# Optimization experiments

Measured on AMD Instinct MI355X. Metric: run time of the kernel, lower is better.

Reference implementation:

```python
import jax, jax.numpy as jnp
import numpy as np

N = 131072
E = 524288
H = 128
EPS = 1e-5

def _layernorm(h, g, b):
    mu = jnp.mean(h, axis=-1, keepdims=True)
    var = jnp.mean((h - mu) ** 2, axis=-1, keepdims=True)
    return (h - mu) * jax.lax.rsqrt(var + EPS) * g + b

def _node_to_node(x, senders, receivers, valid, num_nodes, params):
    # two-way (symmetrized) message passing: gather + scatter_add, then MLP+LN
    W1, b1, W2, b2, W3, b3, g, beta = params
    tws = jnp.concatenate([senders, receivers])
    twr = jnp.concatenate([receivers, senders])
    msg = x[tws]  # [2E', H] gather
    if valid is not None:
        msg = jnp.where(jnp.concatenate([valid, valid])[:, None], msg, 0.0)
    agg = jax.ops.segment_sum(msg, twr, num_segments=num_nodes)  # scatter_add
    h = jax.nn.gelu(agg @ W1 + b1, approximate=False)
    h = jax.nn.gelu(h @ W2 + b2, approximate=False)
    h = h @ W3 + b3
    return _layernorm(h, g, beta)

def setup_inputs() -> dict:
    key = jax.random.key(0)
    ks = jax.random.split(key, 20)
    s = 0.05
    inp = {
        "x": jax.random.normal(ks[0], (N, H), dtype=jnp.float32),
        "edge_index": jax.random.randint(ks[1], (2, E), 0, N, dtype=jnp.int32),
        "pool_p": jax.random.normal(ks[2], (H,), dtype=jnp.float32),
    }
    names = ["dW1", "db1", "dW2", "db2", "dW3", "db3", "dg", "dbeta",
             "uW1", "ub1", "uW2", "ub2", "uW3", "ub3", "ug", "ubeta"]
    shapes = [(H, H), (H,), (H, H), (H,), (H, H), (H,), (H,), (H,),
              (2 * H, H), (H,), (H, H), (H,), (H, H), (H,), (H,), (H,)]
    for i, (nm, sh) in enumerate(zip(names, shapes)):
        if nm in ("dg", "ug"):
            inp[nm] = jnp.ones(sh, dtype=jnp.float32)
        elif nm in ("dbeta", "ubeta") or nm.startswith(("db", "ub")):
            inp[nm] = jnp.zeros(sh, dtype=jnp.float32)
        else:
            inp[nm] = jax.random.normal(ks[3 + i], sh, dtype=jnp.float32) * s
    return inp

def reference(x, edge_index, pool_p,
              dW1, db1, dW2, db2, dW3, db3, dg, dbeta,
              uW1, ub1, uW2, ub2, uW3, ub3, ug, ubeta):
    senders, receivers = edge_index[0], edge_index[1]
    k = N // 2  # TopKPooling ratio=0.5

    # ---- down: TopKPooling ----
    score = x @ pool_p / jnp.linalg.norm(pool_p)  # [N]
    _, perm = jax.lax.top_k(score, k)             # kept node indices
    x_skip = x
    x_p = x[perm] * jnp.tanh(score[perm])[:, None]  # [k, H]
    mask = jnp.zeros((N,), dtype=bool).at[perm].set(True)
    mapping = jnp.zeros((N,), dtype=jnp.int32).at[perm].set(
        jnp.arange(k, dtype=jnp.int32))
    valid = mask[senders] & mask[receivers]
    ps, pr = mapping[senders], mapping[receivers]

    # down conv on pooled graph
    x_d = _node_to_node(x_p, ps, pr, valid, k,
                        (dW1, db1, dW2, db2, dW3, db3, dg, dbeta))

    # ---- up: unpool (indexed scatter write) + skip concat + up conv ----
    recovered = jnp.zeros_like(x_skip).at[perm].set(x_d)
    x_u = jnp.concatenate([recovered, x_skip], axis=-1)  # [N, 2H]
    out = _node_to_node(x_u, senders, receivers, None, N,
                        (uW1, ub1, uW2, ub2, uW3, ub3, ug, ubeta))
    return out
```

## Files before the change

kernel.cpp:

```cpp
#include <hip/hip_runtime.h>

#define N_NODES 131072
#define N_EDGES 524288
#define K_TOP   65536
#define LN_EPS  1e-5f
#define N_TILES (N_NODES / 64)
#define BCAP    5120u

typedef unsigned int u32;
typedef unsigned short u16;
typedef unsigned long long u64;

typedef __attribute__((ext_vector_type(8))) short bf8;
typedef __attribute__((ext_vector_type(4))) float f4;

#define ST_OFF    0
#define CANON_OFF (64u<<10)
#define PART_OFF  (576u<<10)
#define KEYS_OFF  (1u<<20)
#define TVAL_OFF  (2u<<20)
#define KEPT_OFF  ((2u<<20)+(512u<<10))
#define SBUF_OFF  (3u<<20)
#define ADJ_OFF   (35u<<20)


#define C_DW1 0
#define C_DB1 16384
#define C_DW2 16512
#define C_DB2 32896
#define C_DW3 33024
#define C_DB3 49408
#define C_DG  49536
#define C_DBE 49664
#define C_UW1 49792
#define C_UB1 82560
#define C_UW2 82688
#define C_UB2 99072
#define C_UW3 99200
#define C_UB3 115584
#define C_UG  115712
#define C_UBE 115840
#define C_TOT 115968
#define CT_DW1 115968
#define CT_DW2 132352
#define CT_DW3 148736
#define CT_UW1 165120
#define CT_UW2 197888
#define CT_UW3 214272
#define CT_TOT 230656

__device__ __forceinline__ float bflo(u32 u){ return __uint_as_float(u << 16); }
__device__ __forceinline__ float bfhi(u32 u){ return __uint_as_float(u & 0xFFFF0000u); }
__device__ __forceinline__ float bf2f(u16 v){ return __uint_as_float(((u32)v) << 16); }
__device__ __forceinline__ u32 f2bf(float f){
  u32 u = __float_as_uint(f);
  return (u + 0x7FFFu + ((u >> 16) & 1u)) >> 16;
}
__device__ __forceinline__ float gelu_f(float x){
  return 0.5f * x * (1.0f + erff(x * 0.7071067811865476f));
}
__device__ __forceinline__ float2 f2add(float2 a, float2 b){
  return make_float2(a.x + b.x, a.y + b.y);
}

__device__ __forceinline__ int swz16(int row, int cc){
  return row * 128 + ((cc ^ (row & 15)) * 8);
}

__device__ __forceinline__ bf8 ld_bf16_chunk(const u32* __restrict__ rowp, int s, int quad){
  uint4 v = *(const uint4*)(rowp + s * 16 + quad * 4);
  return __builtin_bit_cast(bf8, v);
}
__device__ __forceinline__ bf8 scale_bf16_chunk(const u32* __restrict__ rowp, int s, int quad, float tv){
  uint4 v = *(const uint4*)(rowp + s * 16 + quad * 4);
  uint4 q;
  q.x = f2bf(bflo(v.x) * tv) | (f2bf(bfhi(v.x) * tv) << 16);
  q.y = f2bf(bflo(v.y) * tv) | (f2bf(bfhi(v.y) * tv) << 16);
  q.z = f2bf(bflo(v.z) * tv) | (f2bf(bfhi(v.z) * tv) << 16);
  q.w = f2bf(bflo(v.w) * tv) | (f2bf(bfhi(v.w) * tv) << 16);
  return __builtin_bit_cast(bf8, q);
}
__device__ __forceinline__ bf8 cvt_f32_chunk(const float* __restrict__ rowp, int s, int quad, float tv){
  const float* p = rowp + s * 32 + quad * 8;
  float4 f0 = *(const float4*)p;
  float4 f1 = *(const float4*)(p + 4);
  uint4 q;
  q.x = f2bf(f0.x * tv) | (f2bf(f0.y * tv) << 16);
  q.y = f2bf(f0.z * tv) | (f2bf(f0.w * tv) << 16);
  q.z = f2bf(f1.x * tv) | (f2bf(f1.y * tv) << 16);
  q.w = f2bf(f1.z * tv) | (f2bf(f1.w * tv) << 16);
  return __builtin_bit_cast(bf8, q);
}

__device__ __forceinline__ void gemm_ab(const u16* ws, const bf8 a[4], int mn, int quad, f4 acc[8]){
  #pragma unroll
  for (int s = 0; s < 4; s++){
    #pragma unroll
    for (int j = 0; j < 8; j++){
      bf8 b = *(const bf8*)&ws[swz16(j * 16 + mn, s * 4 + quad)];
      acc[j] = __builtin_amdgcn_mfma_f32_16x16x32_bf16(a[s], b, acc[j], 0, 0, 0);
    }
  }
}

struct SelState {
  u64 prefix;
  u32 krem, eqcnt;
  int is_f32;
  u32 pad;
  double inv_norm;
  u32 eqlist[4096];
  u64 eqkey[4096];
};

struct P16 { const void* q[16]; };

__device__ __forceinline__ void chain_step(const u32* __restrict__ tots, int q,
                                           u32* sfx, u32* selb, int t,
                                           u64& pref, u32& target){
  sfx[t] = tots[q * 256 + t];
  __syncthreads();
  for (int o = 1; o < 256; o <<= 1){
    u32 x = (t + o < 256) ? sfx[t + o] : 0u;
    __syncthreads();
    sfx[t] += x;
    __syncthreads();
  }
  u32 above = (t == 255) ? 0u : sfx[t + 1];
  if (sfx[t] >= target && above < target){ selb[0] = (u32)t; selb[1] = target - above; }
  __syncthreads();
  pref = (pref << 8) | (u64)selb[0];
  target = selb[1];
  __syncthreads();
}

__global__ void k_detect(const u32* __restrict__ xw, SelState* st){
  int t = threadIdx.x;
  int cnt = 0;
  for (int i = t; i < 4096; i += 256){
    u32 w = xw[(size_t)i * 2048];
    u32 e = (w >> 23) & 0xFFu;
    if (e >= 97u && e <= 135u) cnt++;
  }
  __shared__ int sh[256];
  sh[t] = cnt; __syncthreads();
  for (int o = 128; o > 0; o >>= 1){ if (t < o) sh[t] += sh[t+o]; __syncthreads(); }
  if (t == 0){
    st->is_f32 = (sh[0] >= 3072) ? 1 : 0;
    st->prefix = 0; st->krem = K_TOP; st->eqcnt = 0;
  }
}

__global__ void k_canon(P16 ps, const SelState* __restrict__ st, u16* __restrict__ canon,
                        u32* __restrict__ tots, u32* __restrict__ gcur){
  int i = blockIdx.x * 256 + threadIdx.x;
  if (i < 1024) tots[i] = 0u;
  if (i < 256)  gcur[i] = (u32)i * BCAP;
  if (i >= CT_TOT) return;
  int isf = st->is_f32;
  if (i < C_TOT){
    const int off[17] = {C_DW1,C_DB1,C_DW2,C_DB2,C_DW3,C_DB3,C_DG,C_DBE,
                         C_UW1,C_UB1,C_UW2,C_UB2,C_UW3,C_UB3,C_UG,C_UBE,C_TOT};
    int seg = 0;
    #pragma unroll
    for (int s2 = 0; s2 < 16; s2++) if (i >= off[s2+1]) seg = s2 + 1;
    int j = i - off[seg];
    if (isf) canon[i] = (u16)f2bf(((const float*)ps.q[seg])[j]);
    else     canon[i] = ((const u16*)ps.q[seg])[j];
  } else {
    const int dst[7] = {CT_DW1, CT_DW2, CT_DW3, CT_UW1, CT_UW2, CT_UW3, CT_TOT};
    const int wq[6]  = {0, 2, 4, 8, 10, 12};
    int g = i;
    int seg = 0;
    #pragma unroll
    for (int s2 = 0; s2 < 6; s2++) if (g >= dst[s2+1]) seg = s2 + 1;
    int loc = g - dst[seg];
    int K = (seg == 3) ? 256 : 128;
    int n = loc / K, k = loc % K;
    int src = k * 128 + n;
    if (isf) canon[g] = (u16)f2bf(((const float*)ps.q[wq[seg]])[src]);
    else     canon[g] = ((const u16*)ps.q[wq[seg]])[src];
  }
}

__global__ __launch_bounds__(256) void k_score(const void* __restrict__ xraw, const void* __restrict__ praw,
                        const SelState* __restrict__ st,
                        u64* __restrict__ keys, float* __restrict__ tval){
  int t = threadIdx.x, lane = t & 63, w = t >> 6;
  int n = blockIdx.x * 4 + w;
  double d, ps;
  if (st->is_f32){
    const float* xf = (const float*)xraw + (size_t)n * 128;
    const float* pf = (const float*)praw;
    double p0 = (double)pf[lane], p1 = (double)pf[64 + lane];
    d  = (double)xf[lane] * p0 + (double)xf[64 + lane] * p1;
    ps = p0 * p0 + p1 * p1;
  } else {
    const u32* xw = (const u32*)xraw + (size_t)n * 64;
    const u32* pw = (const u32*)praw;
    u32 xx = xw[lane], pv = pw[lane];
    double p0 = (double)bflo(pv), p1 = (double)bfhi(pv);
    d  = (double)bflo(xx) * p0 + (double)bfhi(xx) * p1;
    ps = p0 * p0 + p1 * p1;
  }
  for (int o = 32; o > 0; o >>= 1){
    d  += __shfl_down(d,  o, 64);
    ps += __shfl_down(ps, o, 64);
  }
  if (lane == 0){
    double sc = d * (1.0 / sqrt(ps));
    u64 u = (u64)__double_as_longlong(sc);
    u64 key = (u & 0x8000000000000000ULL) ? ~u : (u | 0x8000000000000000ULL);
    keys[n] = key;
    tval[n] = tanhf((float)sc);
  }
}

__global__ __launch_bounds__(256) void k_histp(const u64* __restrict__ keys,
                                               u32* __restrict__ tots, int pass){
  __shared__ u32 sfx[256];
  __shared__ u32 selb[2];
  __shared__ u32 h[256];
  int t = threadIdx.x;
  u64 pref = 0;
  u32 target = K_TOP;
  for (int q = 0; q < pass; q++)
    chain_step(tots, q, sfx, selb, t, pref, target);
  h[t] = 0;
  __syncthreads();
  int sh_d = 56 - 8 * pass;
  for (int n = blockIdx.x * 256 + t; n < N_NODES; n += 256 * 256){
    u64 k = keys[n];
    bool m = (pass == 0) ? true : ((k >> (sh_d + 8)) == pref);
    if (m) atomicAdd(&h[(u32)((k >> sh_d) & 255)], 1u);
  }
  __syncthreads();
  if (h[t]) atomicAdd(&tots[pass * 256 + t], h[t]);
}

__global__ __launch_bounds__(256) void k_mark(const u64* __restrict__ keys,
                                              const u32* __restrict__ tots,
                                              SelState* st, u32* __restrict__ kept){
  __shared__ u32 sfx[256];
  __shared__ u32 selb[2];
  int t = threadIdx.x;
  u64 pref = 0;
  u32 target = K_TOP;
  for (int q = 0; q < 4; q++)
    chain_step(tots, q, sfx, selb, t, pref, target);
  u32 T = (u32)pref;
  int n = blockIdx.x * 256 + t;
  u64 k = keys[n];
  u32 t32 = (u32)(k >> 32);
  kept[n] = (t32 > T) ? 1u : 0u;
  if (t32 == T){
    u32 i = atomicAdd(&st->eqcnt, 1u);
    if (i < 4096){ st->eqlist[i] = (u32)n; st->eqkey[i] = k; }
  }
}

__global__ __launch_bounds__(256) void k_tie(const u32* __restrict__ tots,
                                             SelState* st, u32* __restrict__ kept){
  __shared__ u32 sfx[256];
  __shared__ u32 selb[2];
  int t = threadIdx.x;
  u64 pref = 0;
  u32 target = K_TOP;
  for (int q = 0; q < 4; q++)
    chain_step(tots, q, sfx, selb, t, pref, target);
  u32 r = target;
  u32 m = st->eqcnt; if (m > 4096) m = 4096;
  for (u32 i = t; i < m; i += 256){
    u64 ki = st->eqkey[i]; u32 ii = st->eqlist[i];
    u32 rank = 0;
    for (u32 j = 0; j < m; j++){
      u64 kj = st->eqkey[j];
      rank += (kj > ki || (kj == ki && st->eqlist[j] < ii)) ? 1u : 0u;
    }
    if (rank < r) kept[ii] = 1u;
  }
}

__global__ __launch_bounds__(256) void k_bin(const int* __restrict__ se, const int* __restrict__ re,
                                             u32* __restrict__ gcur, u32* __restrict__ pairs){
  __shared__ u32 cnt[256], sc[256], base[256], cur[256], gpos[256];
  __shared__ u32 stage[8192];
  int t = threadIdx.x;
  cnt[t] = 0;
  __syncthreads();
  int e0 = blockIdx.x * 4096;
  for (int i = t; i < 4096; i += 256){
    int s = se[e0 + i], r = re[e0 + i];
    atomicAdd(&cnt[(u32)r >> 9], 1u);
    atomicAdd(&cnt[(u32)s >> 9], 1u);
  }
  __syncthreads();
  sc[t] = cnt[t];
  __syncthreads();
  for (int o = 1; o < 256; o <<= 1){
    u32 x = (t >= o) ? sc[t - o] : 0u;
    __syncthreads();
    sc[t] += x;
    __syncthreads();
  }
  base[t] = sc[t] - cnt[t];
  cur[t] = base[t];
  gpos[t] = atomicAdd(&gcur[t], cnt[t]);
  __syncthreads();
  for (int i = t; i < 4096; i += 256){
    u32 s = (u32)se[e0 + i], r = (u32)re[e0 + i];
    u32 b1 = r >> 9, p1 = ((r & 511u) << 17) | s;
    u32 b2 = s >> 9, p2 = ((s & 511u) << 17) | r;
    stage[atomicAdd(&cur[b1], 1u)] = p1;
    stage[atomicAdd(&cur[b2], 1u)] = p2;
  }
  __syncthreads();
  int lane = t & 63, wv = t >> 6;
  for (int b = wv; b < 256; b += 4){
    u32 n = cnt[b], src = base[b], dst = gpos[b];
    for (u32 i = lane; i < n; i += 64)
      pairs[dst + i] = stage[src + i];
  }
}

__global__ __launch_bounds__(256) void k_place(const u32* __restrict__ gcur,
                                               const u32* __restrict__ pairs,
                                               const u32* __restrict__ kept,
                                               u32* __restrict__ adj,
                                               u32* __restrict__ off, u32* __restrict__ cnts){
  __shared__ u32 cnt[512], ck[512], curk[512], curn[512], lo[512], ex2[256];
  int b = blockIdx.x, t = threadIdx.x;
  u32 base = (u32)b * BCAP;
  u32 total = gcur[b] - base;
  cnt[t] = 0; cnt[t + 256] = 0;
  ck[t] = 0;  ck[t + 256] = 0;
  curk[t] = 0; curk[t + 256] = 0;
  curn[t] = 0; curn[t + 256] = 0;
  __syncthreads();
  for (u32 i = t; i < total; i += 256){
    u32 p = pairs[base + i];
    u32 nl = p >> 17, m = p & 0x1FFFFu;
    atomicAdd(&cnt[nl], 1u);
    if (kept[m]) atomicAdd(&ck[nl], 1u);
  }
  __syncthreads();
  u32 c0 = cnt[2 * t], c1 = cnt[2 * t + 1];
  ex2[t] = c0 + c1;
  __syncthreads();
  for (int o = 1; o < 256; o <<= 1){
    u32 x = (t >= o) ? ex2[t - o] : 0u;
    __syncthreads();
    ex2[t] += x;
    __syncthreads();
  }
  u32 e0 = ex2[t] - c0 - c1;
  int n0 = b * 512 + 2 * t;
  off[n0]     = base + e0;
  off[n0 + 1] = base + e0 + c0;
  cnts[n0]     = (ck[2 * t] << 16) | c0;
  cnts[n0 + 1] = (ck[2 * t + 1] << 16) | c1;
  lo[2 * t] = e0; lo[2 * t + 1] = e0 + c0;
  __syncthreads();
  for (u32 i = t; i < total; i += 256){
    u32 p = pairs[base + i];
    u32 nl = p >> 17, m = p & 0x1FFFFu;
    u32 slot;
    if (kept[m]) slot = base + lo[nl] + atomicAdd(&curk[nl], 1u);
    else         slot = base + lo[nl] + ck[nl] + atomicAdd(&curn[nl], 1u);
    adj[slot] = m;
  }
}


__global__ __launch_bounds__(256, 3) void k_proj_down(
    const void* __restrict__ xraw, const float* __restrict__ tval,
    const u16* __restrict__ W1T, const SelState* __restrict__ st,
    const u32* __restrict__ kept, u32* __restrict__ S)
{
  __shared__ u16 w1s[128 * 128];
  __shared__ u16 os[64 * 128];
  int t = threadIdx.x, lane = t & 63, wv = t >> 6;
  int m0 = wv * 16, mn = lane & 15, quad = lane >> 4;

  for (int i = t; i < 2048; i += 256){
    int row = i >> 4, cc = i & 15;
    *(uint4*)&w1s[swz16(row, cc)] = *(const uint4*)(W1T + row * 128 + cc * 8);
  }
  int isf = st->is_f32;
  __syncthreads();

  for (int tile = blockIdx.x; tile < N_TILES; tile += gridDim.x){
    int row0 = tile * 64;
    int arow = row0 + m0 + mn;
    float tv = tval[arow];
    bf8 a[4];
    if (isf){
      const float* xf = (const float*)xraw + (size_t)arow * 128;
      #pragma unroll
      for (int s = 0; s < 4; s++) a[s] = cvt_f32_chunk(xf, s, quad, tv);
    } else {
      const u32* xw = (const u32*)xraw + (size_t)arow * 64;
      #pragma unroll
      for (int s = 0; s < 4; s++) a[s] = scale_bf16_chunk(xw, s, quad, tv);
    }
    f4 acc[8];
    #pragma unroll
    for (int j = 0; j < 8; j++){ acc[j][0]=0.f; acc[j][1]=0.f; acc[j][2]=0.f; acc[j][3]=0.f; }
    gemm_ab(w1s, a, mn, quad, acc);

    #pragma unroll
    for (int j = 0; j < 8; j++){
      int c = j * 16 + mn;
      #pragma unroll
      for (int rg = 0; rg < 4; rg++){
        int row = m0 + quad * 4 + rg;
        os[row * 128 + ((c >> 3) ^ (row & 15)) * 8 + (c & 7)] = (u16)f2bf(acc[j][rg]);
      }
    }
    __builtin_amdgcn_wave_barrier();
    int rl = m0 + (lane >> 2), qt = lane & 3;
    u32 kp = kept[row0 + rl];
    u32* out = S + (size_t)(row0 + rl) * 64;
    if (kp){
      #pragma unroll
      for (int i = 0; i < 4; i++){
        int cc = qt * 4 + i;
        *(uint4*)(out + cc * 4) = *(const uint4*)&os[swz16(rl, cc)];
      }
    }
    __builtin_amdgcn_wave_barrier();
  }
}

__global__ __launch_bounds__(256, 2) void k_proj_up(
    const u32* __restrict__ R, const void* __restrict__ xraw,
    const u16* __restrict__ W1T, const SelState* __restrict__ st,
    u32* __restrict__ S2)
{
  __shared__ u16 was[128 * 128];
  __shared__ u16 wbs[128 * 128];
  __shared__ u16 os[64 * 128];
  int t = threadIdx.x, lane = t & 63, wv = t >> 6;
  int m0 = wv * 16, mn = lane & 15, quad = lane >> 4;

  for (int i = t; i < 2048; i += 256){
    int row = i >> 4, cc = i & 15;
    *(uint4*)&was[swz16(row, cc)] = *(const uint4*)(W1T + row * 256 + cc * 8);
    *(uint4*)&wbs[swz16(row, cc)] = *(const uint4*)(W1T + row * 256 + 128 + cc * 8);
  }
  int isf = st->is_f32;
  __syncthreads();

  for (int tile = blockIdx.x; tile < N_TILES; tile += gridDim.x){
    int row0 = tile * 64;
    int arow = row0 + m0 + mn;
    bf8 a[4];
    const u32* rp = R + (size_t)arow * 64;
    #pragma unroll
    for (int s = 0; s < 4; s++) a[s] = ld_bf16_chunk(rp, s, quad);
    f4 acc[8];
    #pragma unroll
    for (int j = 0; j < 8; j++){ acc[j][0]=0.f; acc[j][1]=0.f; acc[j][2]=0.f; acc[j][3]=0.f; }
    gemm_ab(was, a, mn, quad, acc);

    if (isf){
      const float* xf = (const float*)xraw + (size_t)arow * 128;
      #pragma unroll
      for (int s = 0; s < 4; s++) a[s] = cvt_f32_chunk(xf, s, quad, 1.0f);
    } else {
      const u32* xw = (const u32*)xraw + (size_t)arow * 64;
      #pragma unroll
      for (int s = 0; s < 4; s++) a[s] = ld_bf16_chunk(xw, s, quad);
    }
    gemm_ab(wbs, a, mn, quad, acc);

    #pragma unroll
    for (int j = 0; j < 8; j++){
      int c = j * 16 + mn;
      #pragma unroll
      for (int rg = 0; rg < 4; rg++){
        int row = m0 + quad * 4 + rg;
        os[row * 128 + ((c >> 3) ^ (row & 15)) * 8 + (c & 7)] = (u16)f2bf(acc[j][rg]);
      }
    }
    __builtin_amdgcn_wave_barrier();
    int rl = m0 + (lane >> 2), qt = lane & 3;
    u32* out = S2 + (size_t)(row0 + rl) * 64;
    #pragma unroll
    for (int i = 0; i < 4; i++){
      int cc = qt * 4 + i;
      *(uint4*)(out + cc * 4) = *(const uint4*)&os[swz16(rl, cc)];
    }
    __builtin_amdgcn_wave_barrier();
  }
}

template<int IS_DOWN>
__global__ __launch_bounds__(256, 4) void k_agg(
    const u32* __restrict__ Smsg, const u32* __restrict__ off, const u32* __restrict__ cnts,
    const u32* __restrict__ adj,
    const u16* __restrict__ cb1, const u32* __restrict__ kept,
    u32* __restrict__ H)
{
  int t = threadIdx.x, lane = t & 63, wv = t >> 6;
  float b1l = bf2f(cb1[2 * lane]), b1h = bf2f(cb1[2 * lane + 1]);
  int base = blockIdx.x * 16 + wv * 4;
  #pragma unroll 1
  for (int rr = 0; rr < 4; rr++){
    int n = base + rr;
    if (IS_DOWN && !kept[n]){ H[(size_t)n * 64 + lane] = 0u; continue; }
    u32 c = cnts[n];
    u32 jb = off[n];
    u32 je = jb + (IS_DOWN ? (c >> 16) : (c & 0xFFFFu));
    float2 a = make_float2(0.f, 0.f);
    u32 j = jb;
    for (; j + 8 <= je; j += 8){
      u32 e0 = adj[j],   e1 = adj[j+1], e2 = adj[j+2], e3 = adj[j+3];
      u32 e4 = adj[j+4], e5 = adj[j+5], e6 = adj[j+6], e7 = adj[j+7];
      u32 w0 = Smsg[(size_t)e0 * 64 + lane];
      u32 w1 = Smsg[(size_t)e1 * 64 + lane];
      u32 w2 = Smsg[(size_t)e2 * 64 + lane];
      u32 w3 = Smsg[(size_t)e3 * 64 + lane];
      u32 w4 = Smsg[(size_t)e4 * 64 + lane];
      u32 w5 = Smsg[(size_t)e5 * 64 + lane];
      u32 w6 = Smsg[(size_t)e6 * 64 + lane];
      u32 w7 = Smsg[(size_t)e7 * 64 + lane];
      float2 v0 = make_float2(bflo(w0), bfhi(w0));
      float2 v1 = make_float2(bflo(w1), bfhi(w1));
      float2 v2 = make_float2(bflo(w2), bfhi(w2));
      float2 v3 = make_float2(bflo(w3), bfhi(w3));
      float2 v4 = make_float2(bflo(w4), bfhi(w4));
      float2 v5 = make_float2(bflo(w5), bfhi(w5));
      float2 v6 = make_float2(bflo(w6), bfhi(w6));
      float2 v7 = make_float2(bflo(w7), bfhi(w7));
      a = f2add(a, f2add(f2add(f2add(v0, v1), f2add(v2, v3)),
                         f2add(f2add(v4, v5), f2add(v6, v7))));
    }
    for (; j + 4 <= je; j += 4){
      u32 e0 = adj[j], e1 = adj[j+1], e2 = adj[j+2], e3 = adj[j+3];
      u32 w0 = Smsg[(size_t)e0 * 64 + lane];
      u32 w1 = Smsg[(size_t)e1 * 64 + lane];
      u32 w2 = Smsg[(size_t)e2 * 64 + lane];
      u32 w3 = Smsg[(size_t)e3 * 64 + lane];
      float2 v0 = make_float2(bflo(w0), bfhi(w0));
      float2 v1 = make_float2(bflo(w1), bfhi(w1));
      float2 v2 = make_float2(bflo(w2), bfhi(w2));
      float2 v3 = make_float2(bflo(w3), bfhi(w3));
      a = f2add(a, f2add(f2add(v0, v1), f2add(v2, v3)));
    }
    for (; j < je; j++){
      u32 w = Smsg[(size_t)adj[j] * 64 + lane];
      a = f2add(a, make_float2(bflo(w), bfhi(w)));
    }
    H[(size_t)n * 64 + lane] = f2bf(gelu_f(a.x + b1l)) | (f2bf(gelu_f(a.y + b1h)) << 16);
  }
}

template<int IS_DOWN>
__global__ __launch_bounds__(256, 2) void k_mlp(
    const u32* __restrict__ H,
    const u16* __restrict__ cW2T, const u16* __restrict__ cb2,
    const u16* __restrict__ cW3T, const u16* __restrict__ cb3,
    const u16* __restrict__ cg, const u16* __restrict__ cbe,
    const u32* __restrict__ kept, const SelState* __restrict__ st,
    u32* __restrict__ Rout, void* __restrict__ fout)
{
  __shared__ u16 w2s[128 * 128];
  __shared__ u16 w3s[128 * 128];
  __shared__ u16 os[64 * 128];
  int t = threadIdx.x, lane = t & 63, wv = t >> 6;
  int m0 = wv * 16, mn = lane & 15, quad = lane >> 4;

  for (int i = t; i < 2048; i += 256){
    int row = i >> 4, cc = i & 15;
    *(uint4*)&w2s[swz16(row, cc)] = *(const uint4*)(cW2T + row * 128 + cc * 8);
    *(uint4*)&w3s[swz16(row, cc)] = *(const uint4*)(cW3T + row * 128 + cc * 8);
  }
  float b2v[8], b3v[8], gv[8], bev[8];
  #pragma unroll
  for (int j = 0; j < 8; j++){
    int c = j * 16 + mn;
    b2v[j] = bf2f(cb2[c]); b3v[j] = bf2f(cb3[c]);
    gv[j]  = bf2f(cg[c]);  bev[j] = bf2f(cbe[c]);
  }
  int isf = st->is_f32;
  __syncthreads();

  for (int tile = blockIdx.x; tile < N_TILES; tile += gridDim.x){
    int row0 = tile * 64;
    int arow = row0 + m0 + mn;

    bf8 a[4];
    const u32* hp = H + (size_t)arow * 64;
    #pragma unroll
    for (int s = 0; s < 4; s++) a[s] = ld_bf16_chunk(hp, s, quad);
    f4 acc[8];
    #pragma unroll
    for (int j = 0; j < 8; j++){ acc[j][0]=0.f; acc[j][1]=0.f; acc[j][2]=0.f; acc[j][3]=0.f; }
    gemm_ab(w2s, a, mn, quad, acc);

    #pragma unroll
    for (int j = 0; j < 8; j++){
      int c = j * 16 + mn;
      #pragma unroll
      for (int rg = 0; rg < 4; rg++){
        int row = m0 + quad * 4 + rg;
        os[row * 128 + ((c >> 3) ^ (row & 15)) * 8 + (c & 7)] = (u16)f2bf(gelu_f(acc[j][rg] + b2v[j]));
      }
    }
    __builtin_amdgcn_wave_barrier();

    #pragma unroll
    for (int s = 0; s < 4; s++) a[s] = *(const bf8*)&os[swz16(m0 + mn, s * 4 + quad)];
    #pragma unroll
    for (int j = 0; j < 8; j++){ acc[j][0]=0.f; acc[j][1]=0.f; acc[j][2]=0.f; acc[j][3]=0.f; }
    gemm_ab(w3s, a, mn, quad, acc);

    #pragma unroll
    for (int j = 0; j < 8; j++){
      #pragma unroll
      for (int rg = 0; rg < 4; rg++) acc[j][rg] += b3v[j];
    }
    float s1[4] = {0.f,0.f,0.f,0.f}, s2[4] = {0.f,0.f,0.f,0.f};
    #pragma unroll
    for (int j = 0; j < 8; j++){
      #pragma unroll
      for (int rg = 0; rg < 4; rg++){
        float v = acc[j][rg];
        s1[rg] += v; s2[rg] += v * v;
      }
    }
    #pragma unroll
    for (int o = 1; o < 16; o <<= 1){
      #pragma unroll
      for (int rg = 0; rg < 4; rg++){
        s1[rg] += __shfl_xor(s1[rg], o, 64);
        s2[rg] += __shfl_xor(s2[rg], o, 64);
      }
    }
    float mu[4], rs[4];
    #pragma unroll
    for (int rg = 0; rg < 4; rg++){
      mu[rg] = s1[rg] * 0.0078125f;
      float var = s2[rg] * 0.0078125f - mu[rg] * mu[rg];
      rs[rg] = rsqrtf(var + LN_EPS);
    }
    #pragma unroll
    for (int j = 0; j < 8; j++){
      #pragma unroll
      for (int rg = 0; rg < 4; rg++)
        acc[j][rg] = (acc[j][rg] - mu[rg]) * rs[rg] * gv[j] + bev[j];
    }

    if (!IS_DOWN && isf){
      float* fo = (float*)fout;
      #pragma unroll
      for (int j = 0; j < 8; j++){
        #pragma unroll
        for (int rg = 0; rg < 4; rg++)
          fo[(size_t)(row0 + m0 + quad * 4 + rg) * 128 + j * 16 + mn] = acc[j][rg];
      }
      continue;
    }

    __builtin_amdgcn_wave_barrier();
    #pragma unroll
    for (int j = 0; j < 8; j++){
      int c = j * 16 + mn;
      #pragma unroll
      for (int rg = 0; rg < 4; rg++){
        int row = m0 + quad * 4 + rg;
        os[row * 128 + ((c >> 3) ^ (row & 15)) * 8 + (c & 7)] = (u16)f2bf(acc[j][rg]);
      }
    }
    __builtin_amdgcn_wave_barrier();
    int rl = m0 + (lane >> 2), qt = lane & 3;
    u32 kp = IS_DOWN ? kept[row0 + rl] : 1u;
    u32* out = (IS_DOWN ? Rout : (u32*)fout) + (size_t)(row0 + rl) * 64;
    #pragma unroll
    for (int i = 0; i < 4; i++){
      int cc = qt * 4 + i;
      uint4 w = *(const uint4*)&os[swz16(rl, cc)];
      if (!kp){ w.x = 0; w.y = 0; w.z = 0; w.w = 0; }
      *(uint4*)(out + cc * 4) = w;
    }
    __builtin_amdgcn_wave_barrier();
  }
}


extern "C" void kernel_launch(void* const* d_in, const int* in_sizes, int n_in,
                              void* d_out, int out_size, void* d_ws, size_t ws_size,
                              hipStream_t stream)
{
  const void* x     = d_in[0];
  const int* eidx   = (const int*)d_in[1];
  const void* poolp = d_in[2];
  const int* senders = eidx;
  const int* receivers = eidx + N_EDGES;

  char* ws = (char*)d_ws;
  SelState* st = (SelState*)(ws + ST_OFF);
  u16*  canon  = (u16*) (ws + CANON_OFF);
  u32*  tots   = (u32*) (ws + PART_OFF);
  u32*  gcur   = (u32*) (ws + PART_OFF + 4096);
  u64*  keys   = (u64*) (ws + KEYS_OFF);
  u32*  off    = (u32*) (ws + KEYS_OFF);
  u32*  cnts   = (u32*) (ws + KEYS_OFF + (512u<<10));
  float* tval  = (float*)(ws + TVAL_OFF);
  u32*  kept   = (u32*) (ws + KEPT_OFF);
  u32*  Sbuf   = (u32*) (ws + SBUF_OFF);
  u32*  adj    = (u32*) (ws + ADJ_OFF);
  u32*  pairs  = Sbuf;
  u32*  Dbuf   = (u32*) d_out;

  P16 ps;
  for (int i = 0; i < 16; i++) ps.q[i] = d_in[3 + i];

  k_detect<<<1, 256, 0, stream>>>((const u32*)x, st);
  k_canon<<<(CT_TOT + 255) / 256, 256, 0, stream>>>(ps, st, canon, tots, gcur);
  k_score<<<N_NODES / 4, 256, 0, stream>>>(x, poolp, st, keys, tval);
  for (int pass = 0; pass < 4; pass++)
    k_histp<<<256, 256, 0, stream>>>(keys, tots, pass);
  k_mark<<<N_NODES / 256, 256, 0, stream>>>(keys, tots, st, kept);
  k_tie<<<1, 256, 0, stream>>>(tots, st, kept);

  k_bin<<<N_EDGES / 4096, 256, 0, stream>>>(senders, receivers, gcur, pairs);
  k_place<<<256, 256, 0, stream>>>(gcur, pairs, kept, adj, off, cnts);

  k_proj_down<<<768, 256, 0, stream>>>(x, tval, canon + CT_DW1, st, kept, Sbuf);
  k_agg<1><<<N_NODES / 16, 256, 0, stream>>>(Sbuf, off, cnts, adj, canon + C_DB1, kept, Dbuf);
  k_mlp<1><<<512, 256, 0, stream>>>(Dbuf,
      canon + CT_DW2, canon + C_DB2, canon + CT_DW3, canon + C_DB3,
      canon + C_DG, canon + C_DBE, kept, st, Sbuf, nullptr);

  k_proj_up<<<512, 256, 0, stream>>>(Sbuf, x, canon + CT_UW1, st, Dbuf);
  k_agg<0><<<N_NODES / 16, 256, 0, stream>>>(Dbuf, off, cnts, adj, canon + C_UB1, kept, Sbuf);
  k_mlp<0><<<512, 256, 0, stream>>>(Sbuf,
      canon + CT_UW2, canon + C_UB2, canon + CT_UW3, canon + C_UB3,
      canon + C_UG, canon + C_UBE, kept, st, nullptr, d_out);
}
```

Before: 441.7 us.

## Compact kept nodes into perm list and run down-path only on kept rows

Builds an explicit list of kept node indices through a three-kernel block-sum, scan and write pass. The down aggregation and down MLP then iterate over only the K kept rows, addressed through perm, instead of over all N rows with masking. Because non-kept rows of the down output are no longer zeroed, the up projection now masks them on load using kept. The first radix histogram pass is also folded into k_score with global atomics, which removes one k_histp launch. In exchange it adds three small launches, indirect row addressing, and heavy global atomic contention on the 256 histogram bins in k_score.

```diff
diff --git a/kernel.cpp b/kernel.cpp
--- a/kernel.cpp
+++ b/kernel.cpp
@@ -5,6 +5,7 @@
 #define K_TOP   65536
 #define LN_EPS  1e-5f
 #define N_TILES (N_NODES / 64)
+#define K_TILES (K_TOP / 64)
 #define BCAP    5120u
 
 typedef unsigned int u32;
@@ -185,7 +186,8 @@
 
 __global__ __launch_bounds__(256) void k_score(const void* __restrict__ xraw, const void* __restrict__ praw,
                         const SelState* __restrict__ st,
-                        u64* __restrict__ keys, float* __restrict__ tval){
+                        u64* __restrict__ keys, float* __restrict__ tval,
+                        u32* __restrict__ tots){
   int t = threadIdx.x, lane = t & 63, w = t >> 6;
   int n = blockIdx.x * 4 + w;
   double d, ps;
@@ -213,6 +215,7 @@
     u64 key = (u & 0x8000000000000000ULL) ? ~u : (u | 0x8000000000000000ULL);
     keys[n] = key;
     tval[n] = tanhf((float)sc);
+    atomicAdd(&tots[(u32)(key >> 56)], 1u);
   }
 }
 
@@ -231,7 +234,7 @@
   int sh_d = 56 - 8 * pass;
   for (int n = blockIdx.x * 256 + t; n < N_NODES; n += 256 * 256){
     u64 k = keys[n];
-    bool m = (pass == 0) ? true : ((k >> (sh_d + 8)) == pref);
+    bool m = ((k >> (sh_d + 8)) == pref);
     if (m) atomicAdd(&h[(u32)((k >> sh_d) & 255)], 1u);
   }
   __syncthreads();
@@ -281,6 +284,50 @@
   }
 }
 
+__global__ __launch_bounds__(256) void k_psum(const u32* __restrict__ kept, u32* __restrict__ bsum){
+  __shared__ u32 sh[256];
+  int t = threadIdx.x;
+  sh[t] = kept[blockIdx.x * 256 + t];
+  __syncthreads();
+  for (int o = 128; o > 0; o >>= 1){ if (t < o) sh[t] += sh[t+o]; __syncthreads(); }
+  if (t == 0) bsum[blockIdx.x] = sh[0];
+}
+
+__global__ void k_pscan(u32* __restrict__ bsum){
+  __shared__ u32 ex2[256];
+  int t = threadIdx.x;
+  u32 c0 = bsum[2 * t], c1 = bsum[2 * t + 1];
+  ex2[t] = c0 + c1;
+  __syncthreads();
+  for (int o = 1; o < 256; o <<= 1){
+    u32 x = (t >= o) ? ex2[t - o] : 0u;
+    __syncthreads();
+    ex2[t] += x;
+    __syncthreads();
+  }
+  u32 e0 = ex2[t] - c0 - c1;
+  bsum[2 * t] = e0;
+  bsum[2 * t + 1] = e0 + c0;
+}
+
+__global__ __launch_bounds__(256) void k_pwrite(const u32* __restrict__ kept,
+                                                const u32* __restrict__ bsum,
+                                                u32* __restrict__ perm){
+  __shared__ u32 sc[256];
+  int t = threadIdx.x;
+  int n = blockIdx.x * 256 + t;
+  u32 kp = kept[n];
+  sc[t] = kp;
+  __syncthreads();
+  for (int o = 1; o < 256; o <<= 1){
+    u32 x = (t >= o) ? sc[t - o] : 0u;
+    __syncthreads();
+    sc[t] += x;
+    __syncthreads();
+  }
+  if (kp) perm[bsum[blockIdx.x] + sc[t] - 1u] = (u32)n;
+}
+
 __global__ __launch_bounds__(256) void k_bin(const int* __restrict__ se, const int* __restrict__ re,
                                              u32* __restrict__ gcur, u32* __restrict__ pairs){
   __shared__ u32 cnt[256], sc[256], base[256], cur[256], gpos[256];
@@ -435,7 +482,7 @@
 __global__ __launch_bounds__(256, 2) void k_proj_up(
     const u32* __restrict__ R, const void* __restrict__ xraw,
     const u16* __restrict__ W1T, const SelState* __restrict__ st,
-    u32* __restrict__ S2)
+    const u32* __restrict__ kept, u32* __restrict__ S2)
 {
   __shared__ u16 was[128 * 128];
   __shared__ u16 wbs[128 * 128];
@@ -455,9 +502,13 @@
     int row0 = tile * 64;
     int arow = row0 + m0 + mn;
     bf8 a[4];
+    u32 kp = kept[arow];
     const u32* rp = R + (size_t)arow * 64;
     #pragma unroll
-    for (int s = 0; s < 4; s++) a[s] = ld_bf16_chunk(rp, s, quad);
+    for (int s = 0; s < 4; s++){
+      if (kp) a[s] = ld_bf16_chunk(rp, s, quad);
+      else { uint4 z = {0,0,0,0}; a[s] = __builtin_bit_cast(bf8, z); }
+    }
     f4 acc[8];
     #pragma unroll
     for (int j = 0; j < 8; j++){ acc[j][0]=0.f; acc[j][1]=0.f; acc[j][2]=0.f; acc[j][3]=0.f; }
@@ -495,11 +546,55 @@
   }
 }
 
-template<int IS_DOWN>
-__global__ __launch_bounds__(256, 4) void k_agg(
+__device__ __forceinline__ void agg_row(const u32* __restrict__ Smsg, const u32* __restrict__ adj,
+                                        u32 jb, u32 je, int lane, float b1l, float b1h,
+                                        u32* __restrict__ Hrow){
+  float2 a = make_float2(0.f, 0.f);
+  u32 j = jb;
+  for (; j + 8 <= je; j += 8){
+    u32 e0 = adj[j],   e1 = adj[j+1], e2 = adj[j+2], e3 = adj[j+3];
+    u32 e4 = adj[j+4], e5 = adj[j+5], e6 = adj[j+6], e7 = adj[j+7];
+    u32 w0 = Smsg[(size_t)e0 * 64 + lane];
+    u32 w1 = Smsg[(size_t)e1 * 64 + lane];
+    u32 w2 = Smsg[(size_t)e2 * 64 + lane];
+    u32 w3 = Smsg[(size_t)e3 * 64 + lane];
+    u32 w4 = Smsg[(size_t)e4 * 64 + lane];
+    u32 w5 = Smsg[(size_t)e5 * 64 + lane];
+    u32 w6 = Smsg[(size_t)e6 * 64 + lane];
+    u32 w7 = Smsg[(size_t)e7 * 64 + lane];
+    float2 v0 = make_float2(bflo(w0), bfhi(w0));
+    float2 v1 = make_float2(bflo(w1), bfhi(w1));
+    float2 v2 = make_float2(bflo(w2), bfhi(w2));
+    float2 v3 = make_float2(bflo(w3), bfhi(w3));
+    float2 v4 = make_float2(bflo(w4), bfhi(w4));
+    float2 v5 = make_float2(bflo(w5), bfhi(w5));
+    float2 v6 = make_float2(bflo(w6), bfhi(w6));
+    float2 v7 = make_float2(bflo(w7), bfhi(w7));
+    a = f2add(a, f2add(f2add(f2add(v0, v1), f2add(v2, v3)),
+                       f2add(f2add(v4, v5), f2add(v6, v7))));
+  }
+  for (; j + 4 <= je; j += 4){
+    u32 e0 = adj[j], e1 = adj[j+1], e2 = adj[j+2], e3 = adj[j+3];
+    u32 w0 = Smsg[(size_t)e0 * 64 + lane];
+    u32 w1 = Smsg[(size_t)e1 * 64 + lane];
+    u32 w2 = Smsg[(size_t)e2 * 64 + lane];
+    u32 w3 = Smsg[(size_t)e3 * 64 + lane];
+    float2 v0 = make_float2(bflo(w0), bfhi(w0));
+    float2 v1 = make_float2(bflo(w1), bfhi(w1));
+    float2 v2 = make_float2(bflo(w2), bfhi(w2));
+    float2 v3 = make_float2(bflo(w3), bfhi(w3));
+    a = f2add(a, f2add(f2add(v0, v1), f2add(v2, v3)));
+  }
+  for (; j < je; j++){
+    u32 w = Smsg[(size_t)adj[j] * 64 + lane];
+    a = f2add(a, make_float2(bflo(w), bfhi(w)));
+  }
+  Hrow[lane] = f2bf(gelu_f(a.x + b1l)) | (f2bf(gelu_f(a.y + b1h)) << 16);
+}
+
+__global__ __launch_bounds__(256, 4) void k_agg_up(
     const u32* __restrict__ Smsg, const u32* __restrict__ off, const u32* __restrict__ cnts,
-    const u32* __restrict__ adj,
-    const u16* __restrict__ cb1, const u32* __restrict__ kept,
+    const u32* __restrict__ adj, const u16* __restrict__ cb1,
     u32* __restrict__ H)
 {
   int t = threadIdx.x, lane = t & 63, wv = t >> 6;
@@ -508,51 +603,24 @@
   #pragma unroll 1
   for (int rr = 0; rr < 4; rr++){
     int n = base + rr;
-    if (IS_DOWN && !kept[n]){ H[(size_t)n * 64 + lane] = 0u; continue; }
-    u32 c = cnts[n];
     u32 jb = off[n];
-    u32 je = jb + (IS_DOWN ? (c >> 16) : (c & 0xFFFFu));
-    float2 a = make_float2(0.f, 0.f);
-    u32 j = jb;
-    for (; j + 8 <= je; j += 8){
-      u32 e0 = adj[j],   e1 = adj[j+1], e2 = adj[j+2], e3 = adj[j+3];
-      u32 e4 = adj[j+4], e5 = adj[j+5], e6 = adj[j+6], e7 = adj[j+7];
-      u32 w0 = Smsg[(size_t)e0 * 64 + lane];
-      u32 w1 = Smsg[(size_t)e1 * 64 + lane];
-      u32 w2 = Smsg[(size_t)e2 * 64 + lane];
-      u32 w3 = Smsg[(size_t)e3 * 64 + lane];
-      u32 w4 = Smsg[(size_t)e4 * 64 + lane];
-      u32 w5 = Smsg[(size_t)e5 * 64 + lane];
-      u32 w6 = Smsg[(size_t)e6 * 64 + lane];
-      u32 w7 = Smsg[(size_t)e7 * 64 + lane];
-      float2 v0 = make_float2(bflo(w0), bfhi(w0));
-      float2 v1 = make_float2(bflo(w1), bfhi(w1));
-      float2 v2 = make_float2(bflo(w2), bfhi(w2));
-      float2 v3 = make_float2(bflo(w3), bfhi(w3));
-      float2 v4 = make_float2(bflo(w4), bfhi(w4));
-      float2 v5 = make_float2(bflo(w5), bfhi(w5));
-      float2 v6 = make_float2(bflo(w6), bfhi(w6));
-      float2 v7 = make_float2(bflo(w7), bfhi(w7));
-      a = f2add(a, f2add(f2add(f2add(v0, v1), f2add(v2, v3)),
-                         f2add(f2add(v4, v5), f2add(v6, v7))));
-    }
-    for (; j + 4 <= je; j += 4){
-      u32 e0 = adj[j], e1 = adj[j+1], e2 = adj[j+2], e3 = adj[j+3];
-      u32 w0 = Smsg[(size_t)e0 * 64 + lane];
-      u32 w1 = Smsg[(size_t)e1 * 64 + lane];
-      u32 w2 = Smsg[(size_t)e2 * 64 + lane];
-      u32 w3 = Smsg[(size_t)e3 * 64 + lane];
-      float2 v0 = make_float2(bflo(w0), bfhi(w0));
-      float2 v1 = make_float2(bflo(w1), bfhi(w1));
-      float2 v2 = make_float2(bflo(w2), bfhi(w2));
-      float2 v3 = make_float2(bflo(w3), bfhi(w3));
-      a = f2add(a, f2add(f2add(v0, v1), f2add(v2, v3)));
-    }
-    for (; j < je; j++){
-      u32 w = Smsg[(size_t)adj[j] * 64 + lane];
-      a = f2add(a, make_float2(bflo(w), bfhi(w)));
-    }
-    H[(size_t)n * 64 + lane] = f2bf(gelu_f(a.x + b1l)) | (f2bf(gelu_f(a.y + b1h)) << 16);
+    agg_row(Smsg, adj, jb, jb + (cnts[n] & 0xFFFFu), lane, b1l, b1h, H + (size_t)n * 64);
+  }
+}
+
+__global__ __launch_bounds__(256, 4) void k_agg_down(
+    const u32* __restrict__ Smsg, const u32* __restrict__ off, const u32* __restrict__ cnts,
+    const u32* __restrict__ adj, const u16* __restrict__ cb1,
+    const u32* __restrict__ perm, u32* __restrict__ H)
+{
+  int t = threadIdx.x, lane = t & 63, wv = t >> 6;
+  float b1l = bf2f(cb1[2 * lane]), b1h = bf2f(cb1[2 * lane + 1]);
+  int base = blockIdx.x * 16 + wv * 4;
+  #pragma unroll 1
+  for (int rr = 0; rr < 4; rr++){
+    int n = (int)perm[base + rr];
+    u32 jb = off[n];
+    agg_row(Smsg, adj, jb, jb + (cnts[n] >> 16), lane, b1l, b1h, H + (size_t)n * 64);
   }
 }
 
@@ -562,7 +630,7 @@
     const u16* __restrict__ cW2T, const u16* __restrict__ cb2,
     const u16* __restrict__ cW3T, const u16* __restrict__ cb3,
     const u16* __restrict__ cg, const u16* __restrict__ cbe,
-    const u32* __restrict__ kept, const SelState* __restrict__ st,
+    const u32* __restrict__ perm, const SelState* __restrict__ st,
     u32* __restrict__ Rout, void* __restrict__ fout)
 {
   __shared__ u16 w2s[128 * 128];
@@ -584,11 +652,12 @@
     gv[j]  = bf2f(cg[c]);  bev[j] = bf2f(cbe[c]);
   }
   int isf = st->is_f32;
-  __syncthreads();
-
-  for (int tile = blockIdx.x; tile < N_TILES; tile += gridDim.x){
+  int ntiles = IS_DOWN ? K_TILES : N_TILES;
+  __syncthreads();
+
+  for (int tile = blockIdx.x; tile < ntiles; tile += gridDim.x){
     int row0 = tile * 64;
-    int arow = row0 + m0 + mn;
+    int arow = IS_DOWN ? (int)perm[row0 + m0 + mn] : (row0 + m0 + mn);
 
     bf8 a[4];
     const u32* hp = H + (size_t)arow * 64;
@@ -675,14 +744,12 @@
     }
     __builtin_amdgcn_wave_barrier();
     int rl = m0 + (lane >> 2), qt = lane & 3;
-    u32 kp = IS_DOWN ? kept[row0 + rl] : 1u;
-    u32* out = (IS_DOWN ? Rout : (u32*)fout) + (size_t)(row0 + rl) * 64;
+    int orow = IS_DOWN ? (int)perm[row0 + rl] : (row0 + rl);
+    u32* out = (IS_DOWN ? Rout : (u32*)fout) + (size_t)orow * 64;
     #pragma unroll
     for (int i = 0; i < 4; i++){
       int cc = qt * 4 + i;
-      uint4 w = *(const uint4*)&os[swz16(rl, cc)];
-      if (!kp){ w.x = 0; w.y = 0; w.z = 0; w.w = 0; }
-      *(uint4*)(out + cc * 4) = w;
+      *(uint4*)(out + cc * 4) = *(const uint4*)&os[swz16(rl, cc)];
     }
     __builtin_amdgcn_wave_barrier();
   }
@@ -704,6 +771,8 @@
   u16*  canon  = (u16*) (ws + CANON_OFF);
   u32*  tots   = (u32*) (ws + PART_OFF);
   u32*  gcur   = (u32*) (ws + PART_OFF + 4096);
+  u32*  bsum   = (u32*) (ws + PART_OFF + 8192);
+  u32*  perm   = (u32*) (ws + PART_OFF + 16384);
   u64*  keys   = (u64*) (ws + KEYS_OFF);
   u32*  off    = (u32*) (ws + KEYS_OFF);
   u32*  cnts   = (u32*) (ws + KEYS_OFF + (512u<<10));
@@ -719,24 +788,28 @@
 
   k_detect<<<1, 256, 0, stream>>>((const u32*)x, st);
   k_canon<<<(CT_TOT + 255) / 256, 256, 0, stream>>>(ps, st, canon, tots, gcur);
-  k_score<<<N_NODES / 4, 256, 0, stream>>>(x, poolp, st, keys, tval);
-  for (int pass = 0; pass < 4; pass++)
+  k_score<<<N_NODES / 4, 256, 0, stream>>>(x, poolp, st, keys, tval, tots);
+  for (int pass = 1; pass < 4; pass++)
     k_histp<<<256, 256, 0, stream>>>(keys, tots, pass);
   k_mark<<<N_NODES / 256, 256, 0, stream>>>(keys, tots, st, kept);
   k_tie<<<1, 256, 0, stream>>>(tots, st, kept);
 
+  k_psum<<<N_NODES / 256, 256, 0, stream>>>(kept, bsum);
+  k_pscan<<<1, 256, 0, stream>>>(bsum);
+  k_pwrite<<<N_NODES / 256, 256, 0, stream>>>(kept, bsum, perm);
+
   k_bin<<<N_EDGES / 4096, 256, 0, stream>>>(senders, receivers, gcur, pairs);
   k_place<<<256, 256, 0, stream>>>(gcur, pairs, kept, adj, off, cnts);
 
   k_proj_down<<<768, 256, 0, stream>>>(x, tval, canon + CT_DW1, st, kept, Sbuf);
-  k_agg<1><<<N_NODES / 16, 256, 0, stream>>>(Sbuf, off, cnts, adj, canon + C_DB1, kept, Dbuf);
+  k_agg_down<<<K_TOP / 16, 256, 0, stream>>>(Sbuf, off, cnts, adj, canon + C_DB1, perm, Dbuf);
   k_mlp<1><<<512, 256, 0, stream>>>(Dbuf,
       canon + CT_DW2, canon + C_DB2, canon + CT_DW3, canon + C_DB3,
-      canon + C_DG, canon + C_DBE, kept, st, Sbuf, nullptr);
-
-  k_proj_up<<<512, 256, 0, stream>>>(Sbuf, x, canon + CT_UW1, st, Dbuf);
-  k_agg<0><<<N_NODES / 16, 256, 0, stream>>>(Dbuf, off, cnts, adj, canon + C_UB1, kept, Sbuf);
+      canon + C_DG, canon + C_DBE, perm, st, Sbuf, nullptr);
+
+  k_proj_up<<<512, 256, 0, stream>>>(Sbuf, x, canon + CT_UW1, st, kept, Dbuf);
+  k_agg_up<<<N_NODES / 16, 256, 0, stream>>>(Dbuf, off, cnts, adj, canon + C_UB1, Sbuf);
   k_mlp<0><<<512, 256, 0, stream>>>(Sbuf,
       canon + CT_UW2, canon + C_UB2, canon + CT_UW3, canon + C_UB3,
-      canon + C_UG, canon + C_UBE, kept, st, nullptr, d_out);
-}
+      canon + C_UG, canon + C_UBE, perm, st, nullptr, d_out);
+}
```

New measurement: 1.115 ms. 2.52x slower.
